# Performance work log

Measured on AMD Instinct MI355X. Metric: run time of the kernel, lower is better.

The kernel has to match this reference:

```python
import jax, jax.numpy as jnp
import numpy as np


def setup_inputs() -> dict:
    key = jax.random.key(0)
    ks = jax.random.split(key, 8)
    B, C, H, W = 4, 256, 64, 64
    D = C // 8  # query/key dim = 32
    x = jax.random.normal(ks[0], (B, C, H, W), dtype=jnp.float32)
    # 1x1 convs == per-pixel linear maps over channels
    wq = jax.random.normal(ks[1], (D, C), dtype=jnp.float32) * 0.05
    bq = jnp.zeros((D,), dtype=jnp.float32)
    wk = jax.random.normal(ks[2], (D, C), dtype=jnp.float32) * 0.05
    bk = jnp.zeros((D,), dtype=jnp.float32)
    wv = jax.random.normal(ks[3], (C, C), dtype=jnp.float32) * 0.05
    bv = jnp.zeros((C,), dtype=jnp.float32)
    # gamma is initialized to 0 in the original; use a nonzero scalar so the
    # attention path actually contributes to the output / gradients.
    gamma = jnp.array([0.5], dtype=jnp.float32)
    return {"x": x, "wq": wq, "bq": bq, "wk": wk, "bk": bk,
            "wv": wv, "bv": bv, "gamma": gamma}


def reference(x, wq, bq, wk, bk, wv, bv, gamma):
    B, C, H, W = x.shape
    N = H * W
    xf = x.reshape(B, C, N)
    q = jnp.einsum('dc,bcn->bdn', wq, xf) + bq[:, None]   # [B, D, N]
    k = jnp.einsum('dc,bcn->bdn', wk, xf) + bk[:, None]   # [B, D, N]
    v = jnp.einsum('oc,bcn->bon', wv, xf) + bv[:, None]   # [B, C, N]
    # energy[b, i, j] = <q_i, k_j>; softmax over keys j (unscaled, as in source)
    energy = jnp.einsum('bdi,bdj->bij', q, k)             # [B, N, N]
    attn = jax.nn.softmax(energy, axis=-1)
    # out[b, c, j] = sum_i attn[b, i, j] * v[b, c, i]  (transposed aggregation,
    # matching bmm(attention.permute(0,2,1), value.permute(0,2,1)))
    out = jnp.einsum('bij,bci->bcj', attn, v)             # [B, C, N]
    out = out.reshape(B, C, H, W)
    return gamma[0] * out + x
```

## Files before the change

### kernel.cpp

```cpp
#include <hip/hip_runtime.h>

#define NB 4
#define CCH 256
#define NN 4096
#define DD 32

typedef __attribute__((ext_vector_type(8))) short bf16x8;
typedef __attribute__((ext_vector_type(8))) _Float16 f16x8;
typedef __attribute__((ext_vector_type(4))) _Float16 f16x4;
typedef __attribute__((ext_vector_type(2))) __fp16 fp16x2;
typedef __attribute__((ext_vector_type(4))) float f32x4;

#define MFB(a,b,c) __builtin_amdgcn_mfma_f32_16x16x32_bf16(a,b,c,0,0,0)
#define MFH(a,b,c) __builtin_amdgcn_mfma_f32_16x16x32_f16(a,b,c,0,0,0)
#define L2E 1.44269504f

__device__ inline unsigned short f2bf(float f){
    union { float f; unsigned u; } v; v.f = f;
    unsigned r = v.u + 0x7fffu + ((v.u >> 16) & 1u);
    return (unsigned short)(r >> 16);
}
__device__ inline float bfval(unsigned short h){
    union { unsigned u; float f; } v; v.u = ((unsigned)h) << 16; return v.f;
}
__device__ inline float vexp2(float x){
    float r; asm("v_exp_f32 %0, %1" : "=v"(r) : "v"(x)); return r;
}
__device__ inline f16x4 pk4(float p0, float p1, float p2, float p3){
    union { fp16x2 h2[2]; f16x4 v; } u;
    u.h2[0] = __builtin_amdgcn_cvt_pkrtz(p0, p1);
    u.h2[1] = __builtin_amdgcn_cvt_pkrtz(p2, p3);
    return u.v;
}

__global__ __launch_bounds__(256) void proj_qk(
    const float* __restrict__ x,
    const float* __restrict__ wq, const float* __restrict__ bq,
    const float* __restrict__ wk, const float* __restrict__ bk,
    _Float16* __restrict__ q16,
    _Float16* __restrict__ k_hi, _Float16* __restrict__ k_lo)
{
    const int t = threadIdx.x;
    const int w = t >> 6;
    const int l = t & 63;
    const int lr = l & 15, lg = l >> 4;
    const int nb = blockIdx.x;
    const int b  = blockIdx.y;
    const int n0 = nb*64 + w*16;
    const int n  = n0 + lr;

    const float* xb = x + (size_t)b*CCH*NN;

    f32x4 acc[4] = {};

    for (int kc = 0; kc < 8; kc++) {
        const int cbase = kc*32 + lg*8;
        float xv[8];
        #pragma unroll
        for (int e = 0; e < 8; e++)
            xv[e] = xb[(size_t)(cbase + e)*NN + n];
        bf16x8 xh, xl;
        #pragma unroll
        for (int e = 0; e < 8; e++) {
            unsigned short h = f2bf(xv[e]);
            xh[e] = (short)h;
            xl[e] = (short)f2bf(xv[e] - bfval(h));
        }
        #pragma unroll
        for (int f = 0; f < 4; f++) {
            const float* wrow = (f < 2) ? (wq + (size_t)(f*16 + lr)*CCH)
                                        : (wk + (size_t)((f-2)*16 + lr)*CCH);
            float4 a4 = *(const float4*)(wrow + cbase);
            float4 b4 = *(const float4*)(wrow + cbase + 4);
            float wv8[8] = {a4.x,a4.y,a4.z,a4.w,b4.x,b4.y,b4.z,b4.w};
            bf16x8 wh, wl;
            #pragma unroll
            for (int e = 0; e < 8; e++) {
                unsigned short h = f2bf(wv8[e]);
                wh[e] = (short)h;
                wl[e] = (short)f2bf(wv8[e] - bfval(h));
            }
            acc[f] = MFB(xh, wl, acc[f]);
            acc[f] = MFB(xl, wh, acc[f]);
            acc[f] = MFB(xh, wh, acc[f]);
        }
    }

    #pragma unroll
    for (int f = 0; f < 4; f++) {
        const int d = (f & 1)*16 + lr;
        const bool isq = (f < 2);
        float bias = isq ? bq[d] : bk[d];
        #pragma unroll
        for (int r = 0; r < 4; r++) {
            int nn = n0 + lg*4 + r;
            float val = acc[f][r] + bias;
            size_t a = ((size_t)(b*NN + nn))*DD + d;
            if (isq) {
                q16[a] = (_Float16)val;
            } else {
                _Float16 h = (_Float16)val;
                k_hi[a] = h;
                k_lo[a] = (_Float16)(val - (float)h);
            }
        }
    }
}

__global__ __launch_bounds__(512) void proj_v(
    const float* __restrict__ x,
    const float* __restrict__ wv, const float* __restrict__ bv,
    _Float16* __restrict__ v16)
{
    const int t = threadIdx.x;
    const int w = t >> 6;
    const int cg = w >> 2;
    const int ng = w & 3;
    const int l = t & 63;
    const int lr = l & 15, lg = l >> 4;
    const int ob = blockIdx.x;
    const int nb = blockIdx.y;
    const int b  = blockIdx.z;
    const int n0 = nb*64 + ng*16;
    const int n  = n0 + lr;
    const int cbase0 = ob*128 + cg*64;

    const float* xb = x + (size_t)b*CCH*NN;

    f32x4 acc[4] = {};

    for (int kc = 0; kc < 8; kc++) {
        const int kbase = kc*32 + lg*8;
        float xv[8];
        #pragma unroll
        for (int e = 0; e < 8; e++)
            xv[e] = xb[(size_t)(kbase + e)*NN + n];
        bf16x8 xh, xl;
        #pragma unroll
        for (int e = 0; e < 8; e++) {
            unsigned short h = f2bf(xv[e]);
            xh[e] = (short)h;
            xl[e] = (short)f2bf(xv[e] - bfval(h));
        }
        #pragma unroll
        for (int f = 0; f < 4; f++) {
            const float* wrow = wv + (size_t)(cbase0 + f*16 + lr)*CCH;
            float4 a4 = *(const float4*)(wrow + kbase);
            float4 b4 = *(const float4*)(wrow + kbase + 4);
            float wv8[8] = {a4.x,a4.y,a4.z,a4.w,b4.x,b4.y,b4.z,b4.w};
            bf16x8 wh, wl;
            #pragma unroll
            for (int e = 0; e < 8; e++) {
                unsigned short h = f2bf(wv8[e]);
                wh[e] = (short)h;
                wl[e] = (short)f2bf(wv8[e] - bfval(h));
            }
            acc[f] = MFB(wl, xh, acc[f]);
            acc[f] = MFB(wh, xl, acc[f]);
            acc[f] = MFB(wh, xh, acc[f]);
        }
    }

    const size_t bslice = (size_t)b*(NN/8);
    #pragma unroll
    for (int f = 0; f < 4; f++) {
        #pragma unroll
        for (int r = 0; r < 4; r++) {
            int c = cbase0 + f*16 + lg*4 + r;
            float val = acc[f][r] + bv[c];
            v16[(((bslice + (n >> 3))*CCH + c) << 3) + (n & 7)] = (_Float16)val;
        }
    }
}

__global__ __launch_bounds__(512) void stats_kernel(
    const _Float16* __restrict__ q16,
    const _Float16* __restrict__ kh, const _Float16* __restrict__ kl,
    float* __restrict__ Zp)
{
    __shared__ float zW[8][64];
    const int t = threadIdx.x;
    const int w = t >> 6;
    const int l = t & 63;
    const int lr = l & 15, lg = l >> 4;
    const int it = blockIdx.x;
    const int jc = blockIdx.y;
    const int b  = blockIdx.z;
    const int ibase = it*64;
    const f32x4 zero = {0.f,0.f,0.f,0.f};

    f16x8 qf[4];
    #pragma unroll
    for (int f = 0; f < 4; f++) {
        size_t a = ((size_t)(b*NN + ibase + f*16 + lr))*DD + lg*8;
        qf[f] = *(const f16x8*)(q16 + a);
    }
    float Z[4] = {0.f, 0.f, 0.f, 0.f};

    const size_t k0 = ((size_t)(b*NN + jc*2048 + w*16 + lr))*DD + lg*8;
    const _Float16* kp  = kh + k0;
    const _Float16* klp = kl + k0;

    for (int jt = 0; jt < 16; ++jt) {
        f16x8 kh2 = *(const f16x8*)kp;
        f16x8 kl2 = *(const f16x8*)klp;
        #pragma unroll
        for (int f = 0; f < 4; f++) {
            f32x4 e = MFH(kl2, qf[f], zero);
            e = MFH(kh2, qf[f], e);
            Z[f] += vexp2(e[0]*L2E) + vexp2(e[1]*L2E)
                  + vexp2(e[2]*L2E) + vexp2(e[3]*L2E);
        }
        kp  += 128*DD;
        klp += 128*DD;
    }
    #pragma unroll
    for (int f = 0; f < 4; f++) {
        Z[f] += __shfl_xor(Z[f], 16, 64);
        Z[f] += __shfl_xor(Z[f], 32, 64);
        if (lg == 0) zW[w][f*16 + lr] = Z[f];
    }
    __syncthreads();
    if (t < 64) {
        float z = 0.f;
        #pragma unroll
        for (int w2 = 0; w2 < 8; ++w2) z += zW[w2][t];
        Zp[((size_t)jc*NB + b)*NN + ibase + t] = z;
    }
}

__global__ __launch_bounds__(256) void combine_kernel(
    const float* __restrict__ Zp, float* __restrict__ Sx)
{
    const int idx = blockIdx.x*256 + threadIdx.x;
    Sx[idx] = log2f(Zp[idx] + Zp[(size_t)NB*NN + idx]);
}

__global__ __launch_bounds__(256, 2) void attn_kernel(
    const _Float16* __restrict__ q16,
    const _Float16* __restrict__ kh16, const _Float16* __restrict__ kl16,
    const _Float16* __restrict__ v16,
    const float* __restrict__ Sx,
    const float* __restrict__ x, const float* __restrict__ gamma,
    float* __restrict__ out)
{
    __shared__ __align__(16) f32x4 Rb[4096];

    const int t = threadIdx.x;
    const int wv = t >> 6;
    const int l = t & 63;
    const int lr = l & 15, lg = l >> 4;

    const int lin = blockIdx.x;
    const int slice = lin & 7;
    const int b   = slice >> 1;
    const int ct  = slice & 1;
    const int jt  = lin >> 3;
    const int jbase = jt*64, cbase = ct*128;

    f16x8 kfh[4], kfl[4];
    #pragma unroll
    for (int jf = 0; jf < 4; jf++) {
        size_t a = ((size_t)(b*NN + jbase + jf*16 + lr))*DD + lg*8;
        kfh[jf] = *(const f16x8*)(kh16 + a);
        kfl[jf] = *(const f16x8*)(kl16 + a);
    }

    const float* Sb = Sx + (size_t)b*NN;
    const _Float16* vb = v16 + (size_t)b*(NN/8)*CCH*8;

    const int i0 = wv*1024;

    const int sigma = 8*(lr >> 2) + (lr & 3);
    const _Float16* qpA = q16 + ((size_t)(b*NN + i0 + sigma))*DD + lg*8;
    const _Float16* qpB = qpA + 4*DD;
    const float* spA = Sb + i0 + 8*lg;
    const float* spB = spA + 4;
    const _Float16* vp = vb + (((size_t)(i0/8 + lg)*CCH + cbase + lr) << 3);

    f32x4 acc[4][8] = {};

    #pragma clang loop unroll(disable)
    for (int s = 0; s < 32; ++s) {
        f16x8 qA = *(const f16x8*)qpA;  qpA += 32*DD;
        f16x8 qB = *(const f16x8*)qpB;  qpB += 32*DD;
        float4 sA4 = *(const float4*)spA; spA += 32;
        float4 sB4 = *(const float4*)spB; spB += 32;
        f16x8 vv[8];
        #pragma unroll
        for (int cf = 0; cf < 8; cf++)
            vv[cf] = *(const f16x8*)(vp + cf*128);
        vp += 32*CCH;

        #pragma unroll
        for (int jf = 0; jf < 4; jf++) {
            f32x4 eA = {};
            eA = MFH(qA, kfl[jf], eA);
            eA = MFH(qA, kfh[jf], eA);
            f32x4 eB = {};
            eB = MFH(qB, kfl[jf], eB);
            eB = MFH(qB, kfh[jf], eB);
            union { f16x4 h4[2]; f16x8 h8; } pu;
            pu.h4[0] = pk4(vexp2(fmaf(eA[0], L2E, -sA4.x)),
                           vexp2(fmaf(eA[1], L2E, -sA4.y)),
                           vexp2(fmaf(eA[2], L2E, -sA4.z)),
                           vexp2(fmaf(eA[3], L2E, -sA4.w)));
            pu.h4[1] = pk4(vexp2(fmaf(eB[0], L2E, -sB4.x)),
                           vexp2(fmaf(eB[1], L2E, -sB4.y)),
                           vexp2(fmaf(eB[2], L2E, -sB4.z)),
                           vexp2(fmaf(eB[3], L2E, -sB4.w)));
            f16x8 pa = pu.h8;
            __builtin_amdgcn_s_setprio(1);
            #pragma unroll
            for (int cf = 0; cf < 8; cf++)
                acc[jf][cf] = MFH(pa, vv[cf], acc[jf][cf]);
            __builtin_amdgcn_s_setprio(0);
        }
    }

    if (wv == 2) {
        #pragma unroll
        for (int jf = 0; jf < 4; jf++)
            #pragma unroll
            for (int cf = 0; cf < 8; cf++)
                Rb[((jf*8 + cf) << 6) + l] = acc[jf][cf];
    } else if (wv == 3) {
        #pragma unroll
        for (int jf = 0; jf < 4; jf++)
            #pragma unroll
            for (int cf = 0; cf < 8; cf++)
                Rb[2048 + ((jf*8 + cf) << 6) + l] = acc[jf][cf];
    }
    __syncthreads();
    if (wv == 0) {
        #pragma unroll
        for (int jf = 0; jf < 4; jf++)
            #pragma unroll
            for (int cf = 0; cf < 8; cf++)
                acc[jf][cf] += Rb[((jf*8 + cf) << 6) + l];
    } else if (wv == 1) {
        #pragma unroll
        for (int jf = 0; jf < 4; jf++)
            #pragma unroll
            for (int cf = 0; cf < 8; cf++)
                acc[jf][cf] += Rb[2048 + ((jf*8 + cf) << 6) + l];
    }
    __syncthreads();
    if (wv == 0) {
        #pragma unroll
        for (int cf = 0; cf < 8; cf++) {
            Rb[((0*8 + cf) << 6) + l] = acc[2][cf];
            Rb[((1*8 + cf) << 6) + l] = acc[3][cf];
        }
    } else if (wv == 1) {
        #pragma unroll
        for (int cf = 0; cf < 8; cf++) {
            Rb[2048 + ((0*8 + cf) << 6) + l] = acc[0][cf];
            Rb[2048 + ((1*8 + cf) << 6) + l] = acc[1][cf];
        }
    }
    __syncthreads();

    const float gam = gamma[0];
    if (wv == 0) {
        #pragma unroll
        for (int cf = 0; cf < 8; cf++) {
            {
                f32x4 o = Rb[2048 + ((0*8 + cf) << 6) + l];
                f32x4 a = acc[0][cf];
                a[0]+=o[0]; a[1]+=o[1]; a[2]+=o[2]; a[3]+=o[3];
                const int c = cbase + cf*16 + lr;
                const int j = jbase + 0*16 + lg*4;
                size_t off = ((size_t)(b*CCH + c))*NN + j;
                float4 xv = *(const float4*)(x + off);
                float4 ov;
                ov.x = fmaf(gam, a[0], xv.x);
                ov.y = fmaf(gam, a[1], xv.y);
                ov.z = fmaf(gam, a[2], xv.z);
                ov.w = fmaf(gam, a[3], xv.w);
                *(float4*)(out + off) = ov;
            }
            {
                f32x4 o = Rb[2048 + ((1*8 + cf) << 6) + l];
                f32x4 a = acc[1][cf];
                a[0]+=o[0]; a[1]+=o[1]; a[2]+=o[2]; a[3]+=o[3];
                const int c = cbase + cf*16 + lr;
                const int j = jbase + 1*16 + lg*4;
                size_t off = ((size_t)(b*CCH + c))*NN + j;
                float4 xv = *(const float4*)(x + off);
                float4 ov;
                ov.x = fmaf(gam, a[0], xv.x);
                ov.y = fmaf(gam, a[1], xv.y);
                ov.z = fmaf(gam, a[2], xv.z);
                ov.w = fmaf(gam, a[3], xv.w);
                *(float4*)(out + off) = ov;
            }
        }
    } else if (wv == 1) {
        #pragma unroll
        for (int cf = 0; cf < 8; cf++) {
            {
                f32x4 o = Rb[((0*8 + cf) << 6) + l];
                f32x4 a = acc[2][cf];
                a[0]+=o[0]; a[1]+=o[1]; a[2]+=o[2]; a[3]+=o[3];
                const int c = cbase + cf*16 + lr;
                const int j = jbase + 2*16 + lg*4;
                size_t off = ((size_t)(b*CCH + c))*NN + j;
                float4 xv = *(const float4*)(x + off);
                float4 ov;
                ov.x = fmaf(gam, a[0], xv.x);
                ov.y = fmaf(gam, a[1], xv.y);
                ov.z = fmaf(gam, a[2], xv.z);
                ov.w = fmaf(gam, a[3], xv.w);
                *(float4*)(out + off) = ov;
            }
            {
                f32x4 o = Rb[((1*8 + cf) << 6) + l];
                f32x4 a = acc[3][cf];
                a[0]+=o[0]; a[1]+=o[1]; a[2]+=o[2]; a[3]+=o[3];
                const int c = cbase + cf*16 + lr;
                const int j = jbase + 3*16 + lg*4;
                size_t off = ((size_t)(b*CCH + c))*NN + j;
                float4 xv = *(const float4*)(x + off);
                float4 ov;
                ov.x = fmaf(gam, a[0], xv.x);
                ov.y = fmaf(gam, a[1], xv.y);
                ov.z = fmaf(gam, a[2], xv.z);
                ov.w = fmaf(gam, a[3], xv.w);
                *(float4*)(out + off) = ov;
            }
        }
    }
}

extern "C" void kernel_launch(void* const* d_in, const int* in_sizes, int n_in,
                              void* d_out, int out_size, void* d_ws, size_t ws_size,
                              hipStream_t stream)
{
    (void)in_sizes; (void)n_in; (void)out_size; (void)ws_size;
    const float* x     = (const float*)d_in[0];
    const float* wq    = (const float*)d_in[1];
    const float* bq    = (const float*)d_in[2];
    const float* wk    = (const float*)d_in[3];
    const float* bk    = (const float*)d_in[4];
    const float* wv    = (const float*)d_in[5];
    const float* bv    = (const float*)d_in[6];
    const float* gamma = (const float*)d_in[7];
    float* out = (float*)d_out;

    char* ws = (char*)d_ws;
    _Float16* q16  = (_Float16*)(ws + 0x000000);
    _Float16* k_hi = (_Float16*)(ws + 0x100000);
    _Float16* k_lo = (_Float16*)(ws + 0x200000);
    _Float16* v16  = (_Float16*)(ws + 0x400000);
    float*    Zp   = (float*)   (ws + 0xC00000);
    float*    Sx   = (float*)   (ws + 0xC20000);

    proj_qk<<<dim3(64, 4),    256, 0, stream>>>(x, wq, bq, wk, bk,
                                                q16, k_hi, k_lo);
    proj_v <<<dim3(2, 64, 4), 512, 0, stream>>>(x, wv, bv, v16);
    stats_kernel  <<<dim3(64, 2, 4), 512, 0, stream>>>(q16, k_hi, k_lo, Zp);
    combine_kernel<<<dim3(64),       256, 0, stream>>>(Zp, Sx);
    attn_kernel   <<<dim3(512),      256, 0, stream>>>(
        q16, k_hi, k_lo, v16, Sx, x, gamma, out);
}
```

Measured before the change: 118.6 us.

## Precompute bf16 hi/lo weight splits once; batch exp before PV MFMAs

Adds a prep kernel that splits the q/k/v projection weights into bf16 hi/lo halves once per call, so the projection kernels load packed bf16 vectors instead of reconverting fp32 weights in every block. In the attention kernel, all four exponentiated probability fragments are computed first, then the 32 PV MFMAs are issued in one high-priority batch. The first change adds an extra launch and workspace traffic. The second raises register pressure from holding four fragments but gives longer uninterrupted matrix-instruction runs.

```diff
diff --git a/kernel.cpp b/kernel.cpp
--- a/kernel.cpp
+++ b/kernel.cpp
@@ -33,10 +33,38 @@
     return u.v;
 }
 
+__global__ __launch_bounds__(256) void prep_w(
+    const float* __restrict__ wq, const float* __restrict__ wk,
+    const float* __restrict__ wv,
+    unsigned short* __restrict__ wq_h, unsigned short* __restrict__ wq_l,
+    unsigned short* __restrict__ wk_h, unsigned short* __restrict__ wk_l,
+    unsigned short* __restrict__ wv_h, unsigned short* __restrict__ wv_l)
+{
+    const int idx = blockIdx.x*256 + threadIdx.x;
+    if (idx < 8192) {
+        float v = wq[idx];
+        unsigned short h = f2bf(v);
+        wq_h[idx] = h;
+        wq_l[idx] = f2bf(v - bfval(h));
+        v = wk[idx];
+        h = f2bf(v);
+        wk_h[idx] = h;
+        wk_l[idx] = f2bf(v - bfval(h));
+    }
+    {
+        float v = wv[idx];
+        unsigned short h = f2bf(v);
+        wv_h[idx] = h;
+        wv_l[idx] = f2bf(v - bfval(h));
+    }
+}
+
 __global__ __launch_bounds__(256) void proj_qk(
     const float* __restrict__ x,
-    const float* __restrict__ wq, const float* __restrict__ bq,
-    const float* __restrict__ wk, const float* __restrict__ bk,
+    const unsigned short* __restrict__ wq_h, const unsigned short* __restrict__ wq_l,
+    const float* __restrict__ bq,
+    const unsigned short* __restrict__ wk_h, const unsigned short* __restrict__ wk_l,
+    const float* __restrict__ bk,
     _Float16* __restrict__ q16,
     _Float16* __restrict__ k_hi, _Float16* __restrict__ k_lo)
 {
@@ -68,18 +96,11 @@
         }
         #pragma unroll
         for (int f = 0; f < 4; f++) {
-            const float* wrow = (f < 2) ? (wq + (size_t)(f*16 + lr)*CCH)
-                                        : (wk + (size_t)((f-2)*16 + lr)*CCH);
-            float4 a4 = *(const float4*)(wrow + cbase);
-            float4 b4 = *(const float4*)(wrow + cbase + 4);
-            float wv8[8] = {a4.x,a4.y,a4.z,a4.w,b4.x,b4.y,b4.z,b4.w};
-            bf16x8 wh, wl;
-            #pragma unroll
-            for (int e = 0; e < 8; e++) {
-                unsigned short h = f2bf(wv8[e]);
-                wh[e] = (short)h;
-                wl[e] = (short)f2bf(wv8[e] - bfval(h));
-            }
+            const size_t wo = (size_t)((f & 1)*16 + lr)*CCH + cbase;
+            const unsigned short* wh_p = (f < 2) ? (wq_h + wo) : (wk_h + wo);
+            const unsigned short* wl_p = (f < 2) ? (wq_l + wo) : (wk_l + wo);
+            bf16x8 wh = *(const bf16x8*)wh_p;
+            bf16x8 wl = *(const bf16x8*)wl_p;
             acc[f] = MFB(xh, wl, acc[f]);
             acc[f] = MFB(xl, wh, acc[f]);
             acc[f] = MFB(xh, wh, acc[f]);
@@ -109,7 +130,8 @@
 
 __global__ __launch_bounds__(512) void proj_v(
     const float* __restrict__ x,
-    const float* __restrict__ wv, const float* __restrict__ bv,
+    const unsigned short* __restrict__ wv_h, const unsigned short* __restrict__ wv_l,
+    const float* __restrict__ bv,
     _Float16* __restrict__ v16)
 {
     const int t = threadIdx.x;
@@ -144,17 +166,9 @@
         }
         #pragma unroll
         for (int f = 0; f < 4; f++) {
-            const float* wrow = wv + (size_t)(cbase0 + f*16 + lr)*CCH;
-            float4 a4 = *(const float4*)(wrow + kbase);
-            float4 b4 = *(const float4*)(wrow + kbase + 4);
-            float wv8[8] = {a4.x,a4.y,a4.z,a4.w,b4.x,b4.y,b4.z,b4.w};
-            bf16x8 wh, wl;
-            #pragma unroll
-            for (int e = 0; e < 8; e++) {
-                unsigned short h = f2bf(wv8[e]);
-                wh[e] = (short)h;
-                wl[e] = (short)f2bf(wv8[e] - bfval(h));
-            }
+            const size_t wo = (size_t)(cbase0 + f*16 + lr)*CCH + kbase;
+            bf16x8 wh = *(const bf16x8*)(wv_h + wo);
+            bf16x8 wl = *(const bf16x8*)(wv_l + wo);
             acc[f] = MFB(wl, xh, acc[f]);
             acc[f] = MFB(wh, xl, acc[f]);
             acc[f] = MFB(wh, xh, acc[f]);
@@ -292,6 +306,7 @@
             vv[cf] = *(const f16x8*)(vp + cf*128);
         vp += 32*CCH;
 
+        f16x8 pa[4];
         #pragma unroll
         for (int jf = 0; jf < 4; jf++) {
             f32x4 eA = {};
@@ -309,13 +324,16 @@
                            vexp2(fmaf(eB[1], L2E, -sB4.y)),
                            vexp2(fmaf(eB[2], L2E, -sB4.z)),
                            vexp2(fmaf(eB[3], L2E, -sB4.w)));
-            f16x8 pa = pu.h8;
-            __builtin_amdgcn_s_setprio(1);
+            pa[jf] = pu.h8;
+        }
+
+        __builtin_amdgcn_s_setprio(1);
+        #pragma unroll
+        for (int jf = 0; jf < 4; jf++)
             #pragma unroll
             for (int cf = 0; cf < 8; cf++)
-                acc[jf][cf] = MFH(pa, vv[cf], acc[jf][cf]);
-            __builtin_amdgcn_s_setprio(0);
-        }
+                acc[jf][cf] = MFH(pa[jf], vv[cf], acc[jf][cf]);
+        __builtin_amdgcn_s_setprio(0);
     }
 
     if (wv == 2) {
@@ -455,10 +473,20 @@
     _Float16* v16  = (_Float16*)(ws + 0x400000);
     float*    Zp   = (float*)   (ws + 0xC00000);
     float*    Sx   = (float*)   (ws + 0xC20000);
-
-    proj_qk<<<dim3(64, 4),    256, 0, stream>>>(x, wq, bq, wk, bk,
+    unsigned short* wq_h = (unsigned short*)(ws + 0xC30000);
+    unsigned short* wq_l = (unsigned short*)(ws + 0xC34000);
+    unsigned short* wk_h = (unsigned short*)(ws + 0xC38000);
+    unsigned short* wk_l = (unsigned short*)(ws + 0xC3C000);
+    unsigned short* wv_h = (unsigned short*)(ws + 0xC40000);
+    unsigned short* wv_l = (unsigned short*)(ws + 0xC60000);
+
+    prep_w<<<dim3(256),       256, 0, stream>>>(wq, wk, wv,
+                                                wq_h, wq_l, wk_h, wk_l,
+                                                wv_h, wv_l);
+    proj_qk<<<dim3(64, 4),    256, 0, stream>>>(x, wq_h, wq_l, bq,
+                                                wk_h, wk_l, bk,
                                                 q16, k_hi, k_lo);
-    proj_v <<<dim3(2, 64, 4), 512, 0, stream>>>(x, wv, bv, v16);
+    proj_v <<<dim3(2, 64, 4), 512, 0, stream>>>(x, wv_h, wv_l, bv, v16);
     stats_kernel  <<<dim3(64, 2, 4), 512, 0, stream>>>(q16, k_hi, k_lo, Zp);
     combine_kernel<<<dim3(64),       256, 0, stream>>>(Zp, Sx);
     attn_kernel   <<<dim3(512),      256, 0, stream>>>(
```

After: 121.9 us. 1.03x slower.

## Fuse QK and V projections, drop combine kernel, batch P·V MFMAs

Applied to the files above, without the earlier changes.

The Q/K and V projection kernels become a single launch: blocks with ob<2 compute V and ob==2 compute Q or K, one per group of four waves. The stats kernel now covers all keys in one block instead of splitting them across two blocks, so it writes log2(Z) directly and the separate combine kernel goes away. In the attention loop, all four P fragments are computed first and then the 32 P·V MFMAs run under a single raised priority region. This removes two launches and the partial-sum round trip, but it halves the stats grid parallelism and raises register pressure in the attention kernel.

```diff
diff --git a/kernel.cpp b/kernel.cpp
--- a/kernel.cpp
+++ b/kernel.cpp
@@ -33,142 +33,135 @@
     return u.v;
 }
 
-__global__ __launch_bounds__(256) void proj_qk(
+__global__ __launch_bounds__(512) void proj_fused(
     const float* __restrict__ x,
     const float* __restrict__ wq, const float* __restrict__ bq,
     const float* __restrict__ wk, const float* __restrict__ bk,
+    const float* __restrict__ wv, const float* __restrict__ bv,
     _Float16* __restrict__ q16,
-    _Float16* __restrict__ k_hi, _Float16* __restrict__ k_lo)
-{
-    const int t = threadIdx.x;
-    const int w = t >> 6;
-    const int l = t & 63;
-    const int lr = l & 15, lg = l >> 4;
-    const int nb = blockIdx.x;
-    const int b  = blockIdx.y;
-    const int n0 = nb*64 + w*16;
-    const int n  = n0 + lr;
-
-    const float* xb = x + (size_t)b*CCH*NN;
-
-    f32x4 acc[4] = {};
-
-    for (int kc = 0; kc < 8; kc++) {
-        const int cbase = kc*32 + lg*8;
-        float xv[8];
-        #pragma unroll
-        for (int e = 0; e < 8; e++)
-            xv[e] = xb[(size_t)(cbase + e)*NN + n];
-        bf16x8 xh, xl;
-        #pragma unroll
-        for (int e = 0; e < 8; e++) {
-            unsigned short h = f2bf(xv[e]);
-            xh[e] = (short)h;
-            xl[e] = (short)f2bf(xv[e] - bfval(h));
-        }
-        #pragma unroll
-        for (int f = 0; f < 4; f++) {
-            const float* wrow = (f < 2) ? (wq + (size_t)(f*16 + lr)*CCH)
-                                        : (wk + (size_t)((f-2)*16 + lr)*CCH);
-            float4 a4 = *(const float4*)(wrow + cbase);
-            float4 b4 = *(const float4*)(wrow + cbase + 4);
-            float wv8[8] = {a4.x,a4.y,a4.z,a4.w,b4.x,b4.y,b4.z,b4.w};
-            bf16x8 wh, wl;
-            #pragma unroll
-            for (int e = 0; e < 8; e++) {
-                unsigned short h = f2bf(wv8[e]);
-                wh[e] = (short)h;
-                wl[e] = (short)f2bf(wv8[e] - bfval(h));
-            }
-            acc[f] = MFB(xh, wl, acc[f]);
-            acc[f] = MFB(xl, wh, acc[f]);
-            acc[f] = MFB(xh, wh, acc[f]);
-        }
-    }
-
-    #pragma unroll
-    for (int f = 0; f < 4; f++) {
-        const int d = (f & 1)*16 + lr;
-        const bool isq = (f < 2);
-        float bias = isq ? bq[d] : bk[d];
-        #pragma unroll
-        for (int r = 0; r < 4; r++) {
-            int nn = n0 + lg*4 + r;
-            float val = acc[f][r] + bias;
-            size_t a = ((size_t)(b*NN + nn))*DD + d;
-            if (isq) {
-                q16[a] = (_Float16)val;
-            } else {
-                _Float16 h = (_Float16)val;
-                k_hi[a] = h;
-                k_lo[a] = (_Float16)(val - (float)h);
-            }
-        }
-    }
-}
-
-__global__ __launch_bounds__(512) void proj_v(
-    const float* __restrict__ x,
-    const float* __restrict__ wv, const float* __restrict__ bv,
+    _Float16* __restrict__ k_hi, _Float16* __restrict__ k_lo,
     _Float16* __restrict__ v16)
 {
-    const int t = threadIdx.x;
-    const int w = t >> 6;
-    const int cg = w >> 2;
-    const int ng = w & 3;
-    const int l = t & 63;
-    const int lr = l & 15, lg = l >> 4;
     const int ob = blockIdx.x;
     const int nb = blockIdx.y;
     const int b  = blockIdx.z;
-    const int n0 = nb*64 + ng*16;
-    const int n  = n0 + lr;
-    const int cbase0 = ob*128 + cg*64;
-
+    const int t = threadIdx.x;
+    const int l = t & 63;
+    const int lr = l & 15, lg = l >> 4;
     const float* xb = x + (size_t)b*CCH*NN;
 
-    f32x4 acc[4] = {};
-
-    for (int kc = 0; kc < 8; kc++) {
-        const int kbase = kc*32 + lg*8;
-        float xv[8];
-        #pragma unroll
-        for (int e = 0; e < 8; e++)
-            xv[e] = xb[(size_t)(kbase + e)*NN + n];
-        bf16x8 xh, xl;
-        #pragma unroll
-        for (int e = 0; e < 8; e++) {
-            unsigned short h = f2bf(xv[e]);
-            xh[e] = (short)h;
-            xl[e] = (short)f2bf(xv[e] - bfval(h));
-        }
+    if (ob < 2) {
+        const int w = t >> 6;
+        const int cg = w >> 2;
+        const int ng = w & 3;
+        const int n0 = nb*64 + ng*16;
+        const int n  = n0 + lr;
+        const int cbase0 = ob*128 + cg*64;
+
+        f32x4 acc[4] = {};
+
+        for (int kc = 0; kc < 8; kc++) {
+            const int kbase = kc*32 + lg*8;
+            float xv[8];
+            #pragma unroll
+            for (int e = 0; e < 8; e++)
+                xv[e] = xb[(size_t)(kbase + e)*NN + n];
+            bf16x8 xh, xl;
+            #pragma unroll
+            for (int e = 0; e < 8; e++) {
+                unsigned short h = f2bf(xv[e]);
+                xh[e] = (short)h;
+                xl[e] = (short)f2bf(xv[e] - bfval(h));
+            }
+            #pragma unroll
+            for (int f = 0; f < 4; f++) {
+                const float* wrow = wv + (size_t)(cbase0 + f*16 + lr)*CCH;
+                float4 a4 = *(const float4*)(wrow + kbase);
+                float4 b4 = *(const float4*)(wrow + kbase + 4);
+                float wv8[8] = {a4.x,a4.y,a4.z,a4.w,b4.x,b4.y,b4.z,b4.w};
+                bf16x8 wh, wl;
+                #pragma unroll
+                for (int e = 0; e < 8; e++) {
+                    unsigned short h = f2bf(wv8[e]);
+                    wh[e] = (short)h;
+                    wl[e] = (short)f2bf(wv8[e] - bfval(h));
+                }
+                acc[f] = MFB(wl, xh, acc[f]);
+                acc[f] = MFB(wh, xl, acc[f]);
+                acc[f] = MFB(wh, xh, acc[f]);
+            }
+        }
+
+        const size_t bslice = (size_t)b*(NN/8);
         #pragma unroll
         for (int f = 0; f < 4; f++) {
-            const float* wrow = wv + (size_t)(cbase0 + f*16 + lr)*CCH;
-            float4 a4 = *(const float4*)(wrow + kbase);
-            float4 b4 = *(const float4*)(wrow + kbase + 4);
-            float wv8[8] = {a4.x,a4.y,a4.z,a4.w,b4.x,b4.y,b4.z,b4.w};
-            bf16x8 wh, wl;
+            #pragma unroll
+            for (int r = 0; r < 4; r++) {
+                int c = cbase0 + f*16 + lg*4 + r;
+                float val = acc[f][r] + bv[c];
+                v16[(((bslice + (n >> 3))*CCH + c) << 3) + (n & 7)] =
+                    (_Float16)val;
+            }
+        }
+    } else {
+        const int w = t >> 6;
+        const int fp = w >> 2;
+        const int ng = w & 3;
+        const int n0 = nb*64 + ng*16;
+        const int n  = n0 + lr;
+
+        f32x4 acc[2] = {};
+
+        for (int kc = 0; kc < 8; kc++) {
+            const int cbase = kc*32 + lg*8;
+            float xv[8];
+            #pragma unroll
+            for (int e = 0; e < 8; e++)
+                xv[e] = xb[(size_t)(cbase + e)*NN + n];
+            bf16x8 xh, xl;
             #pragma unroll
             for (int e = 0; e < 8; e++) {
-                unsigned short h = f2bf(wv8[e]);
-                wh[e] = (short)h;
-                wl[e] = (short)f2bf(wv8[e] - bfval(h));
-            }
-            acc[f] = MFB(wl, xh, acc[f]);
-            acc[f] = MFB(wh, xl, acc[f]);
-            acc[f] = MFB(wh, xh, acc[f]);
-        }
-    }
-
-    const size_t bslice = (size_t)b*(NN/8);
-    #pragma unroll
-    for (int f = 0; f < 4; f++) {
-        #pragma unroll
-        for (int r = 0; r < 4; r++) {
-            int c = cbase0 + f*16 + lg*4 + r;
-            float val = acc[f][r] + bv[c];
-            v16[(((bslice + (n >> 3))*CCH + c) << 3) + (n & 7)] = (_Float16)val;
+                unsigned short h = f2bf(xv[e]);
+                xh[e] = (short)h;
+                xl[e] = (short)f2bf(xv[e] - bfval(h));
+            }
+            #pragma unroll
+            for (int fl = 0; fl < 2; fl++) {
+                const float* wrow = (fp == 0 ? wq : wk)
+                                  + (size_t)(fl*16 + lr)*CCH;
+                float4 a4 = *(const float4*)(wrow + cbase);
+                float4 b4 = *(const float4*)(wrow + cbase + 4);
+                float wv8[8] = {a4.x,a4.y,a4.z,a4.w,b4.x,b4.y,b4.z,b4.w};
+                bf16x8 wh, wl;
+                #pragma unroll
+                for (int e = 0; e < 8; e++) {
+                    unsigned short h = f2bf(wv8[e]);
+                    wh[e] = (short)h;
+                    wl[e] = (short)f2bf(wv8[e] - bfval(h));
+                }
+                acc[fl] = MFB(xh, wl, acc[fl]);
+                acc[fl] = MFB(xl, wh, acc[fl]);
+                acc[fl] = MFB(xh, wh, acc[fl]);
+            }
+        }
+
+        #pragma unroll
+        for (int fl = 0; fl < 2; fl++) {
+            const int d = fl*16 + lr;
+            float bias = fp ? bk[d] : bq[d];
+            #pragma unroll
+            for (int r = 0; r < 4; r++) {
+                int nn = n0 + lg*4 + r;
+                float val = acc[fl][r] + bias;
+                size_t a = ((size_t)(b*NN + nn))*DD + d;
+                if (fp == 0) {
+                    q16[a] = (_Float16)val;
+                } else {
+                    _Float16 h = (_Float16)val;
+                    k_hi[a] = h;
+                    k_lo[a] = (_Float16)(val - (float)h);
+                }
+            }
         }
     }
 }
@@ -176,7 +169,7 @@
 __global__ __launch_bounds__(512) void stats_kernel(
     const _Float16* __restrict__ q16,
     const _Float16* __restrict__ kh, const _Float16* __restrict__ kl,
-    float* __restrict__ Zp)
+    float* __restrict__ Sx)
 {
     __shared__ float zW[8][64];
     const int t = threadIdx.x;
@@ -184,8 +177,7 @@
     const int l = t & 63;
     const int lr = l & 15, lg = l >> 4;
     const int it = blockIdx.x;
-    const int jc = blockIdx.y;
-    const int b  = blockIdx.z;
+    const int b  = blockIdx.y;
     const int ibase = it*64;
     const f32x4 zero = {0.f,0.f,0.f,0.f};
 
@@ -197,11 +189,11 @@
     }
     float Z[4] = {0.f, 0.f, 0.f, 0.f};
 
-    const size_t k0 = ((size_t)(b*NN + jc*2048 + w*16 + lr))*DD + lg*8;
+    const size_t k0 = ((size_t)(b*NN + w*16 + lr))*DD + lg*8;
     const _Float16* kp  = kh + k0;
     const _Float16* klp = kl + k0;
 
-    for (int jt = 0; jt < 16; ++jt) {
+    for (int jt = 0; jt < 32; ++jt) {
         f16x8 kh2 = *(const f16x8*)kp;
         f16x8 kl2 = *(const f16x8*)klp;
         #pragma unroll
@@ -225,15 +217,8 @@
         float z = 0.f;
         #pragma unroll
         for (int w2 = 0; w2 < 8; ++w2) z += zW[w2][t];
-        Zp[((size_t)jc*NB + b)*NN + ibase + t] = z;
-    }
-}
-
-__global__ __launch_bounds__(256) void combine_kernel(
-    const float* __restrict__ Zp, float* __restrict__ Sx)
-{
-    const int idx = blockIdx.x*256 + threadIdx.x;
-    Sx[idx] = log2f(Zp[idx] + Zp[(size_t)NB*NN + idx]);
+        Sx[(size_t)b*NN + ibase + t] = log2f(z);
+    }
 }
 
 __global__ __launch_bounds__(256, 2) void attn_kernel(
@@ -292,6 +277,7 @@
             vv[cf] = *(const f16x8*)(vp + cf*128);
         vp += 32*CCH;
 
+        f16x8 pa[4];
         #pragma unroll
         for (int jf = 0; jf < 4; jf++) {
             f32x4 eA = {};
@@ -309,13 +295,16 @@
                            vexp2(fmaf(eB[1], L2E, -sB4.y)),
                            vexp2(fmaf(eB[2], L2E, -sB4.z)),
                            vexp2(fmaf(eB[3], L2E, -sB4.w)));
-            f16x8 pa = pu.h8;
-            __builtin_amdgcn_s_setprio(1);
+            pa[jf] = pu.h8;
+        }
+
+        __builtin_amdgcn_s_setprio(1);
+        #pragma unroll
+        for (int jf = 0; jf < 4; jf++)
             #pragma unroll
             for (int cf = 0; cf < 8; cf++)
-                acc[jf][cf] = MFH(pa, vv[cf], acc[jf][cf]);
-            __builtin_amdgcn_s_setprio(0);
-        }
+                acc[jf][cf] = MFH(pa[jf], vv[cf], acc[jf][cf]);
+        __builtin_amdgcn_s_setprio(0);
     }
 
     if (wv == 2) {
@@ -453,14 +442,11 @@
     _Float16* k_hi = (_Float16*)(ws + 0x100000);
     _Float16* k_lo = (_Float16*)(ws + 0x200000);
     _Float16* v16  = (_Float16*)(ws + 0x400000);
-    float*    Zp   = (float*)   (ws + 0xC00000);
-    float*    Sx   = (float*)   (ws + 0xC20000);
-
-    proj_qk<<<dim3(64, 4),    256, 0, stream>>>(x, wq, bq, wk, bk,
-                                                q16, k_hi, k_lo);
-    proj_v <<<dim3(2, 64, 4), 512, 0, stream>>>(x, wv, bv, v16);
-    stats_kernel  <<<dim3(64, 2, 4), 512, 0, stream>>>(q16, k_hi, k_lo, Zp);
-    combine_kernel<<<dim3(64),       256, 0, stream>>>(Zp, Sx);
-    attn_kernel   <<<dim3(512),      256, 0, stream>>>(
+    float*    Sx   = (float*)   (ws + 0xC00000);
+
+    proj_fused  <<<dim3(3, 64, 4), 512, 0, stream>>>(
+        x, wq, bq, wk, bk, wv, bv, q16, k_hi, k_lo, v16);
+    stats_kernel<<<dim3(64, 4),    512, 0, stream>>>(q16, k_hi, k_lo, Sx);
+    attn_kernel <<<dim3(512),      256, 0, stream>>>(
         q16, k_hi, k_lo, v16, Sx, x, gamma, out);
 }
```

Measured after the change: 132.5 us. 11.7% more time.
